# Kernel tuning notes

Hardware: AMD Instinct MI355X
Metric: run time of the kernel (lower is better)

Reference implementation:

```python
import jax, jax.numpy as jnp
import numpy as np

B, NOBJ, QD, VD = 128, 36, 2400, 2048
N = B * NOBJ
NEG_SLOPE = 0.2


def _edges():
    # fully connected per image, self-loops included (PyG GATConv adds them)
    base = np.arange(NOBJ)
    src = np.repeat(base, NOBJ)
    dst = np.tile(base, NOBJ)
    off = (np.arange(B) * NOBJ)[:, None]
    return np.stack([(src[None] + off).reshape(-1), (dst[None] + off).reshape(-1)])


def setup_inputs() -> dict:
    key = jax.random.key(0)
    ks = jax.random.split(key, 24)
    p = lambda k, shape, fan: jax.random.normal(k, shape, jnp.float32) * (1.0 / np.sqrt(fan))
    inp = {
        "question_embedding": jax.random.normal(ks[0], (B, QD), jnp.float32),
        "object_features": jax.random.normal(ks[1], (N, VD), jnp.float32),
        "edge_index": jnp.asarray(_edges(), jnp.int32),
        "Wq": p(ks[2], (QD, 2048), QD), "bq": jnp.zeros((2048,), jnp.float32),
        "Wv": p(ks[3], (VD, 2048), VD), "bv": jnp.zeros((2048,), jnp.float32),
        "W1": p(ks[4], (2048, 4 * 256), 2048), "a1s": p(ks[5], (4, 256), 256),
        "a1d": p(ks[6], (4, 256), 256), "b1": jnp.zeros((1024,), jnp.float32),
        "W2": p(ks[7], (1024, 4 * 256), 1024), "a2s": p(ks[8], (4, 256), 256),
        "a2d": p(ks[9], (4, 256), 256), "b2": jnp.zeros((1024,), jnp.float32),
        "W3": p(ks[10], (1024, 5 * 512), 1024), "a3s": p(ks[11], (5, 512), 512),
        "a3d": p(ks[12], (5, 512), 512), "b3": jnp.zeros((512,), jnp.float32),
        "batch_size": B, "num_obj": NOBJ,
    }
    return inp


def gat_conv(x, edge_index, W, a_src, a_dst, b, heads, ch, concat):
    n = x.shape[0]
    h = (x @ W).reshape(n, heads, ch)                       # [N,H,C]
    src, dst = edge_index[0], edge_index[1]
    al_s = jnp.einsum('nhc,hc->nh', h, a_src)               # [N,H]
    al_d = jnp.einsum('nhc,hc->nh', h, a_dst)
    e = jax.nn.leaky_relu(al_s[src] + al_d[dst], NEG_SLOPE)  # [E,H]
    # segment softmax over edges sharing a destination node
    e_max = jax.ops.segment_max(e, dst, num_segments=n)
    e = jnp.exp(e - e_max[dst])
    denom = jax.ops.segment_sum(e, dst, num_segments=n)
    alpha = e / (denom[dst] + 1e-16)                        # [E,H]
    msg = h[src] * alpha[:, :, None]                        # [E,H,C]
    out = jax.ops.segment_sum(msg, dst, num_segments=n)     # [N,H,C]
    out = out.reshape(n, heads * ch) if concat else out.mean(axis=1)
    return out + b


def reference(question_embedding, object_features, edge_index,
              Wq, bq, Wv, bv,
              W1, a1s, a1d, b1,
              W2, a2s, a2d, b2,
              W3, a3s, a3d, b3,
              batch_size, num_obj):
    # hadamard fusion of question with per-object features
    q = question_embedding @ Wq + bq                        # [B,2048]
    q = jnp.repeat(q, num_obj, axis=0)                      # [N,2048]
    v = object_features @ Wv + bv
    x = q * v
    g1 = jax.nn.relu(gat_conv(x, edge_index, W1, a1s, a1d, b1, 4, 256, True))
    g2 = jax.nn.relu(gat_conv(g1, edge_index, W2, a2s, a2d, b2, 4, 256, True))
    g2 = g2 + g1                                            # residual
    return gat_conv(g2, edge_index, W3, a3s, a3d, b3, 5, 512, False)
```

## Files before the change

### kernel.cpp

```cpp
#include <hip/hip_runtime.h>
#include <hip/hip_bf16.h>

typedef unsigned short u16;
typedef __bf16 bf16x8 __attribute__((ext_vector_type(8)));
typedef float f32x4 __attribute__((ext_vector_type(4)));

#define B_IMG 128
#define NOBJ  36
#define NNODE (B_IMG * NOBJ)

__device__ __forceinline__ float b2f(u16 u) {
    union { unsigned int i; float f; } v; v.i = ((unsigned int)u) << 16; return v.f;
}
__device__ __forceinline__ u16 f2b(float f) {
    union { float f; unsigned int i; } v; v.f = f;
    unsigned int u = v.i;
    return (u16)((u + 0x7fffu + ((u >> 16) & 1u)) >> 16);
}

__global__ __launch_bounds__(256)
void conv_mat(const float* __restrict__ src, u16* __restrict__ dst, int n4) {
    const int i = blockIdx.x * 256 + threadIdx.x;
    if (i >= n4) return;
    const float4 f = ((const float4*)src)[i];
    ushort4 o; o.x = f2b(f.x); o.y = f2b(f.y); o.z = f2b(f.z); o.w = f2b(f.w);
    ((ushort4*)dst)[i] = o;
}

__global__ __launch_bounds__(256)
void conv_pad_qe(const float* __restrict__ src, u16* __restrict__ dst) {
    const int i = blockIdx.x * 256 + threadIdx.x;
    if (i >= 128 * 2560) return;
    const int r = i / 2560, c = i - r * 2560;
    dst[i] = (c < 2400) ? f2b(src[r * 2400 + c]) : (u16)0;
}

__global__ __launch_bounds__(256)
void transpose_cvt(const float* __restrict__ src, u16* __restrict__ dst, int R, int C) {
    __shared__ u16 tile[32][33];
    const int bx = blockIdx.x * 32, by = blockIdx.y * 32;
    const int tx = threadIdx.x & 31, ty = threadIdx.x >> 5;
    #pragma unroll
    for (int i = ty; i < 32; i += 8)
        tile[i][tx] = f2b(src[(size_t)(by + i) * C + bx + tx]);
    __syncthreads();
    #pragma unroll
    for (int i = ty; i < 32; i += 8) dst[(size_t)(bx + i) * R + by + tx] = tile[tx][i];
}

__global__ __launch_bounds__(256)
void transpose_cvt_padK(const float* __restrict__ src, u16* __restrict__ dst) {
    __shared__ u16 tile[32][33];
    const int bx = blockIdx.x * 32, by = blockIdx.y * 32;
    const int tx = threadIdx.x & 31, ty = threadIdx.x >> 5;
    #pragma unroll
    for (int i = ty; i < 32; i += 8) {
        const int k = by + i;
        tile[i][tx] = (k < 2400) ? f2b(src[(size_t)k * 2048 + bx + tx]) : (u16)0;
    }
    __syncthreads();
    #pragma unroll
    for (int i = ty; i < 32; i += 8) dst[(size_t)(bx + i) * 2560 + by + tx] = tile[tx][i];
}

template<int EPI>
__global__ __launch_bounds__(256, 4)
void gemm_tn(const u16* __restrict__ A, const u16* __restrict__ Bt,
             int M, int N, int K, int kLen,
             float* __restrict__ Cf, u16* __restrict__ Cb,
             const float* __restrict__ bias, const float* __restrict__ qmul)
{
    __shared__ __align__(16) u16 lds[2 * 8192];

    const int t    = threadIdx.x;
    const int lane = t & 63;
    const int wave = t >> 6;
    const int wr = wave >> 1, wc = wave & 1;
    const int quad = lane >> 4, l16 = lane & 15;
    const int rowBase = blockIdx.y * 128;
    const int colBase = blockIdx.x * 128;
    const int k0 = blockIdx.z * kLen;

    const u16* gA0 = A  + (size_t)(rowBase + wave * 32 + (lane >> 2)) * K + k0 + (lane & 3) * 8;
    const u16* gA1 = gA0 + 16 * (size_t)K;
    const u16* gB0 = Bt + (size_t)(colBase + wave * 32 + (lane >> 2)) * K + k0 + (lane & 3) * 8;
    const u16* gB1 = gB0 + 16 * (size_t)K;
    const int ro = wave * 1024;

    int afr[4], bfr[4];
    #pragma unroll
    for (int r = 0; r < 4; r++) afr[r] = (wr * 64 + r * 16 + l16) * 32 + quad * 8;
    #pragma unroll
    for (int c = 0; c < 4; c++) bfr[c] = 4096 + (wc * 64 + c * 16 + l16) * 32 + quad * 8;

    f32x4 acc[4][4];
    #pragma unroll
    for (int r = 0; r < 4; r++)
        #pragma unroll
        for (int c = 0; c < 4; c++)
            acc[r][c] = (f32x4){0.f, 0.f, 0.f, 0.f};

    auto gld = [](const u16* g, u16* s) {
        __builtin_amdgcn_global_load_lds(
            (const __attribute__((address_space(1))) void*)g,
            (__attribute__((address_space(3))) void*)s, 16, 0, 0);
    };
    auto dma_stage = [&](int it, int st) {
        const int kk = it * 32;
        const int bo = st * 8192;
        gld(gA0 + kk, &lds[bo + ro]);
        gld(gA1 + kk, &lds[bo + ro + 512]);
        gld(gB0 + kk, &lds[bo + 4096 + ro]);
        gld(gB1 + kk, &lds[bo + 4096 + ro + 512]);
    };

    const int nIter = kLen >> 5;
    dma_stage(0, 0);

    for (int it = 0; it < nIter; ++it) {
        asm volatile("s_waitcnt vmcnt(0)\n\ts_barrier" ::: "memory");
        if (it + 1 < nIter) dma_stage(it + 1, (it + 1) & 1);
        const int bo = (it & 1) * 8192;
        bf16x8 avf[4], bvf[4];
        #pragma unroll
        for (int r = 0; r < 4; r++) avf[r] = *(const bf16x8*)&lds[bo + afr[r]];
        #pragma unroll
        for (int c = 0; c < 4; c++) bvf[c] = *(const bf16x8*)&lds[bo + bfr[c]];
        #pragma unroll
        for (int r = 0; r < 4; r++)
            #pragma unroll
            for (int c = 0; c < 4; c++)
                acc[r][c] = __builtin_amdgcn_mfma_f32_16x16x32_bf16(avf[r], bvf[c], acc[r][c], 0, 0, 0);
    }

    #pragma unroll
    for (int r = 0; r < 4; r++) {
        const int mBase = rowBase + wr * 64 + r * 16 + quad * 4;
        #pragma unroll
        for (int c = 0; c < 4; c++) {
            const int n = colBase + wc * 64 + c * 16 + l16;
            #pragma unroll
            for (int e = 0; e < 4; e++) {
                const int m = mBase + e;
                float v = acc[r][c][e];
                if (EPI == 1) {
                    Cf[((size_t)blockIdx.z * M + m) * N + n] = v;
                } else if (EPI == 2) {
                    v += bias[n];
                    v *= qmul[(size_t)(m / NOBJ) * N + n];
                    Cb[(size_t)m * N + n] = f2b(v);
                } else {
                    Cb[(size_t)m * N + n] = f2b(v);
                }
            }
        }
    }
}

__global__ __launch_bounds__(256)
void qcombine(const float* __restrict__ p, const float* __restrict__ bias,
              float* __restrict__ q, int MN, int S)
{
    const int i = blockIdx.x * 256 + threadIdx.x;
    float s = 0.f;
    for (int z = 0; z < S; z++) s += p[(size_t)z * MN + i];
    q[i] = s + bias[i & 2047];
}

template<int H, int C>
__global__ __launch_bounds__(H * 64)
void al_kernel(const u16* __restrict__ h, const float* __restrict__ a_s,
               const float* __restrict__ a_d, float* __restrict__ als, float* __restrict__ ald)
{
    const int n = blockIdx.x;
    const int wv = threadIdx.x >> 6, lane = threadIdx.x & 63;
    constexpr int PL = C / 64;
    const u16*   hp  = h   + (size_t)n * (H * C) + wv * C + lane * PL;
    const float* asp = a_s + wv * C + lane * PL;
    const float* adp = a_d + wv * C + lane * PL;
    u16 hb[PL];
    if constexpr (PL == 4) { *(uint2*)hb = *(const uint2*)hp; }
    else                   { *(uint4*)hb = *(const uint4*)hp; }
    float s1 = 0.f, s2 = 0.f;
    #pragma unroll
    for (int i = 0; i < PL; i++) {
        const float hv = b2f(hb[i]);
        s1 += hv * asp[i];
        s2 += hv * adp[i];
    }
    #pragma unroll
    for (int off = 32; off > 0; off >>= 1) {
        s1 += __shfl_down(s1, off);
        s2 += __shfl_down(s2, off);
    }
    if (lane == 0) { als[n * H + wv] = s1; ald[n * H + wv] = s2; }
}

template<int H, bool MEAN>
__global__ __launch_bounds__(64)
void alpha_kernel(const float* __restrict__ als, const float* __restrict__ ald,
                  float* __restrict__ alphaG)
{
    __shared__ float asl[36];
    const int b = blockIdx.y, hd = blockIdx.x;
    const int nb = b * NOBJ;
    const int t = threadIdx.x;
    if (t < 36) asl[t] = als[(nb + t) * H + hd];
    __syncthreads();
    if (t >= 36) return;
    const float ad = ald[(nb + t) * H + hd];
    float row[36];
    float mx = -1e30f;
    #pragma unroll
    for (int s = 0; s < 36; s++) {
        float v = asl[s] + ad; v = (v > 0.f) ? v : 0.2f * v;
        row[s] = v; mx = fmaxf(mx, v);
    }
    float sum = 0.f;
    #pragma unroll
    for (int s = 0; s < 36; s++) { row[s] = expf(row[s] - mx); sum += row[s]; }
    const float inv = (MEAN ? 0.2f : 1.0f) / (sum + 1e-16f);
    float* o = alphaG + (((size_t)b * H + hd) * 36 + t) * 36;
    #pragma unroll
    for (int s = 0; s < 36; s++) o[s] = row[s] * inv;
}

template<int H, int C, int MODE>
__global__ __launch_bounds__(192)
void attn_agg(const u16* __restrict__ h, const float* __restrict__ alphaG,
              const float* __restrict__ bias, const u16* __restrict__ resid,
              u16* __restrict__ outb)
{
    constexpr int NSLAB = C / 64;
    __shared__ __align__(16) u16 hl[36 * 64];
    __shared__ float al[36 * 36];
    const int b = blockIdx.y;
    const int hd = blockIdx.x / NSLAB, sl = blockIdx.x - hd * NSLAB;
    const int nb = b * NOBJ, cb = sl * 64;
    const int t = threadIdx.x;

    for (int e = t; e < 36 * 8; e += 192) {
        const int row = e >> 3, col = (e & 7) * 8;
        *(uint4*)&hl[row * 64 + col] =
            *(const uint4*)&h[(size_t)(nb + row) * (H * C) + hd * C + cb + col];
    }
    const float* ap = alphaG + ((size_t)b * H + hd) * 1296;
    for (int e = t; e < 1296; e += 192) al[e] = ap[e];
    __syncthreads();

    #pragma unroll
    for (int p = 0; p < 3; p++) {
        const int e = p * 192 + t;
        const int d = e >> 4, c4 = (e & 15) * 4;
        float a0 = 0, a1 = 0, a2 = 0, a3 = 0;
        for (int s = 0; s < 36; s++) {
            const float av = al[d * 36 + s];
            const ushort4 hv = *(const ushort4*)&hl[s * 64 + c4];
            a0 += av * b2f(hv.x); a1 += av * b2f(hv.y);
            a2 += av * b2f(hv.z); a3 += av * b2f(hv.w);
        }
        const int n = nb + d;
        const size_t base = (size_t)n * (H * C) + hd * C + cb + c4;
        const int bb = hd * C + cb + c4;
        float v0 = a0 + bias[bb + 0];
        float v1 = a1 + bias[bb + 1];
        float v2 = a2 + bias[bb + 2];
        float v3 = a3 + bias[bb + 3];
        v0 = v0 > 0.f ? v0 : 0.f; v1 = v1 > 0.f ? v1 : 0.f;
        v2 = v2 > 0.f ? v2 : 0.f; v3 = v3 > 0.f ? v3 : 0.f;
        if (MODE == 2) {
            v0 += b2f(resid[base + 0]); v1 += b2f(resid[base + 1]);
            v2 += b2f(resid[base + 2]); v3 += b2f(resid[base + 3]);
        }
        outb[base + 0] = f2b(v0); outb[base + 1] = f2b(v1);
        outb[base + 2] = f2b(v2); outb[base + 3] = f2b(v3);
    }
}

__global__ __launch_bounds__(192)
void attn_agg_mean(const u16* __restrict__ h, const float* __restrict__ alphaG,
                   const float* __restrict__ b3, float* __restrict__ outp)
{
    __shared__ __align__(16) u16 hl[36 * 64];
    __shared__ float al[36 * 36];
    const int b = blockIdx.y, sl = blockIdx.x;
    const int nb = b * NOBJ, cb = sl * 64;
    const int t = threadIdx.x;

    float acc[3][4] = {};
    for (int hd = 0; hd < 5; hd++) {
        if (hd) __syncthreads();
        for (int e = t; e < 36 * 8; e += 192) {
            const int row = e >> 3, col = (e & 7) * 8;
            *(uint4*)&hl[row * 64 + col] =
                *(const uint4*)&h[(size_t)(nb + row) * 2560 + hd * 512 + cb + col];
        }
        const float* ap = alphaG + ((size_t)b * 5 + hd) * 1296;
        for (int e = t; e < 1296; e += 192) al[e] = ap[e];
        __syncthreads();
        #pragma unroll
        for (int p = 0; p < 3; p++) {
            const int e = p * 192 + t;
            const int d = e >> 4, c4 = (e & 15) * 4;
            for (int s = 0; s < 36; s++) {
                const float av = al[d * 36 + s];
                const ushort4 hv = *(const ushort4*)&hl[s * 64 + c4];
                acc[p][0] += av * b2f(hv.x); acc[p][1] += av * b2f(hv.y);
                acc[p][2] += av * b2f(hv.z); acc[p][3] += av * b2f(hv.w);
            }
        }
    }
    #pragma unroll
    for (int p = 0; p < 3; p++) {
        const int e = p * 192 + t;
        const int d = e >> 4, c4 = (e & 15) * 4;
        #pragma unroll
        for (int j = 0; j < 4; j++)
            outp[(size_t)(nb + d) * 512 + cb + c4 + j] = acc[p][j] + b3[cb + c4 + j];
    }
}

extern "C" void kernel_launch(void* const* d_in, const int* in_sizes, int n_in,
                              void* d_out, int out_size, void* d_ws, size_t ws_size,
                              hipStream_t stream)
{
    const float* qe  = (const float*)d_in[0];
    const float* of  = (const float*)d_in[1];
    const float* Wq  = (const float*)d_in[3];
    const float* bq  = (const float*)d_in[4];
    const float* Wv  = (const float*)d_in[5];
    const float* bv  = (const float*)d_in[6];
    const float* W1  = (const float*)d_in[7];
    const float* a1s = (const float*)d_in[8];
    const float* a1d = (const float*)d_in[9];
    const float* b1  = (const float*)d_in[10];
    const float* W2  = (const float*)d_in[11];
    const float* a2s = (const float*)d_in[12];
    const float* a2d = (const float*)d_in[13];
    const float* b2  = (const float*)d_in[14];
    const float* W3  = (const float*)d_in[15];
    const float* a3s = (const float*)d_in[16];
    const float* a3d = (const float*)d_in[17];
    const float* b3  = (const float*)d_in[18];
    float* out = (float*)d_out;
    (void)ws_size; (void)in_sizes; (void)n_in; (void)out_size;

    char* W0 = (char*)d_ws;
    size_t off = 0;
    auto alloc = [&](size_t bytes) -> char* {
        char* p = W0 + off; off += (bytes + 255) & ~(size_t)255; return p;
    };
    u16* qe_c = (u16*)alloc(128ull * 2560 * 2);
    u16* of_c = (u16*)alloc(4608ull * 2048 * 2);
    const size_t szA = 4608ull * 2560 * 2;
    const size_t szB = 4608ull * 1024 * 2;
    const size_t szC = 4608ull * 1024 * 2;
    char* Abase = alloc(szA);
    char* Bbase = alloc(szB);
    char* Cbase = alloc(szC);
    char* Dbase = alloc((size_t)NNODE * 5 * 4 * 2);
    float* alphaG = (float*)alloc(128ull * 5 * 36 * 36 * 4);

    u16*   WqT   = (u16*)Abase;
    float* qpart = (float*)(Abase + 2048ull * 2560 * 2);
    u16*   x     = (u16*)Abase;
    u16*   g1    = (u16*)Abase;
    u16*   h3    = (u16*)Abase;
    u16*   WvT   = (u16*)Bbase;
    float* q     = (float*)(Bbase + 2048ull * 2048 * 2);
    u16*   W1T   = (u16*)Bbase;
    u16*   W2T   = (u16*)Bbase;
    u16*   g2    = (u16*)Bbase;
    u16*   h1    = (u16*)Cbase;
    u16*   h2    = (u16*)Cbase;
    u16*   W3T   = (u16*)Cbase;
    float* als   = (float*)Dbase;
    float* ald   = (float*)(Dbase + (size_t)NNODE * 5 * 4);

    conv_pad_qe<<<(128 * 2560 + 255) / 256, 256, 0, stream>>>(qe, qe_c);
    conv_mat<<<(4608 * 2048 / 4 + 255) / 256, 256, 0, stream>>>(of, of_c, 4608 * 2048 / 4);

    transpose_cvt_padK<<<dim3(64, 80), 256, 0, stream>>>(Wq, WqT);
    gemm_tn<1><<<dim3(16, 1, 5), 256, 0, stream>>>(qe_c, WqT, 128, 2048, 2560, 512,
                                                   qpart, nullptr, nullptr, nullptr);
    qcombine<<<dim3(128 * 2048 / 256), 256, 0, stream>>>(qpart, bq, q, 128 * 2048, 5);

    transpose_cvt<<<dim3(64, 64), 256, 0, stream>>>(Wv, WvT, 2048, 2048);
    gemm_tn<2><<<dim3(16, 36, 1), 256, 0, stream>>>(of_c, WvT, 4608, 2048, 2048, 2048,
                                                    nullptr, x, bv, q);

    transpose_cvt<<<dim3(32, 64), 256, 0, stream>>>(W1, W1T, 2048, 1024);
    gemm_tn<0><<<dim3(8, 36, 1), 256, 0, stream>>>(x, W1T, 4608, 1024, 2048, 2048,
                                                   nullptr, h1, nullptr, nullptr);
    al_kernel<4, 256><<<dim3(NNODE), 256, 0, stream>>>(h1, a1s, a1d, als, ald);
    alpha_kernel<4, false><<<dim3(4, B_IMG), 64, 0, stream>>>(als, ald, alphaG);
    attn_agg<4, 256, 1><<<dim3(16, B_IMG), 192, 0, stream>>>(h1, alphaG, b1, nullptr, g1);

    transpose_cvt<<<dim3(32, 32), 256, 0, stream>>>(W2, W2T, 1024, 1024);
    gemm_tn<0><<<dim3(8, 36, 1), 256, 0, stream>>>(g1, W2T, 4608, 1024, 1024, 1024,
                                                   nullptr, h2, nullptr, nullptr);
    al_kernel<4, 256><<<dim3(NNODE), 256, 0, stream>>>(h2, a2s, a2d, als, ald);
    alpha_kernel<4, false><<<dim3(4, B_IMG), 64, 0, stream>>>(als, ald, alphaG);
    attn_agg<4, 256, 2><<<dim3(16, B_IMG), 192, 0, stream>>>(h2, alphaG, b2, g1, g2);

    transpose_cvt<<<dim3(80, 32), 256, 0, stream>>>(W3, W3T, 1024, 2560);
    gemm_tn<0><<<dim3(20, 36, 1), 256, 0, stream>>>(g2, W3T, 4608, 2560, 1024, 1024,
                                                    nullptr, h3, nullptr, nullptr);
    al_kernel<5, 512><<<dim3(NNODE), 320, 0, stream>>>(h3, a3s, a3d, als, ald);
    alpha_kernel<5, true><<<dim3(5, B_IMG), 64, 0, stream>>>(als, ald, alphaG);
    attn_agg_mean<<<dim3(8, B_IMG), 192, 0, stream>>>(h3, alphaG, b3, out);
}
```

Measured before the change: 475.9 us.

## Triple-buffer GEMM with swizzled LDS, fuse conversion, transpose and attention-logit kernels

The GEMM moves from double to triple buffering, with a deeper prefetch and a partial vmcnt wait, so global loads overlap more with MFMA work. Its LDS layout is XOR-swizzled to reduce bank conflicts on fragment reads. The separate conversion and transpose kernels are merged into combined launches (W1/W2, Wq/Wv), and the per-node logit kernel is fused with the softmax alpha kernel, cutting launch count and intermediate buffers. Occupancy drops from 4 to 3 blocks per CU because of the extra LDS, and W2T now gets a separate workspace region so it can be transposed early.

```diff
diff --git a/kernel.cpp b/kernel.cpp
--- a/kernel.cpp
+++ b/kernel.cpp
@@ -19,58 +19,55 @@
 }
 
 __global__ __launch_bounds__(256)
-void conv_mat(const float* __restrict__ src, u16* __restrict__ dst, int n4) {
-    const int i = blockIdx.x * 256 + threadIdx.x;
-    if (i >= n4) return;
-    const float4 f = ((const float4*)src)[i];
-    ushort4 o; o.x = f2b(f.x); o.y = f2b(f.y); o.z = f2b(f.z); o.w = f2b(f.w);
-    ((ushort4*)dst)[i] = o;
+void conv_all(const float* __restrict__ of, u16* __restrict__ of_c,
+              const float* __restrict__ qe, u16* __restrict__ qe_c)
+{
+    const int bid = blockIdx.x;
+    if (bid < 9216) {
+        const int i = bid * 256 + threadIdx.x;
+        const float4 f = ((const float4*)of)[i];
+        ushort4 o; o.x = f2b(f.x); o.y = f2b(f.y); o.z = f2b(f.z); o.w = f2b(f.w);
+        ((ushort4*)of_c)[i] = o;
+    } else {
+        const int i = (bid - 9216) * 256 + threadIdx.x;
+        const int r = i / 2560, c = i - r * 2560;
+        qe_c[i] = (c < 2400) ? f2b(qe[r * 2400 + c]) : (u16)0;
+    }
 }
 
 __global__ __launch_bounds__(256)
-void conv_pad_qe(const float* __restrict__ src, u16* __restrict__ dst) {
-    const int i = blockIdx.x * 256 + threadIdx.x;
-    if (i >= 128 * 2560) return;
-    const int r = i / 2560, c = i - r * 2560;
-    dst[i] = (c < 2400) ? f2b(src[r * 2400 + c]) : (u16)0;
-}
-
-__global__ __launch_bounds__(256)
-void transpose_cvt(const float* __restrict__ src, u16* __restrict__ dst, int R, int C) {
+void transpose_cvt2(const float* __restrict__ s0, u16* __restrict__ d0,
+                    int Rs0, int Rd0, int C0, int nt0,
+                    const float* __restrict__ s1, u16* __restrict__ d1,
+                    int Rs1, int Rd1, int C1)
+{
     __shared__ u16 tile[32][33];
-    const int bx = blockIdx.x * 32, by = blockIdx.y * 32;
-    const int tx = threadIdx.x & 31, ty = threadIdx.x >> 5;
-    #pragma unroll
-    for (int i = ty; i < 32; i += 8)
-        tile[i][tx] = f2b(src[(size_t)(by + i) * C + bx + tx]);
+    int tb = blockIdx.x;
+    const float* src; u16* dst; int Rs, Rd, C;
+    if (tb < nt0) { src = s0; dst = d0; Rs = Rs0; Rd = Rd0; C = C0; }
+    else { tb -= nt0; src = s1; dst = d1; Rs = Rs1; Rd = Rd1; C = C1; }
+    const int ntx = C >> 5;
+    const int ty = tb / ntx, tx = tb - ty * ntx;
+    const int bx = tx * 32, by = ty * 32;
+    const int lx = threadIdx.x & 31, ly = threadIdx.x >> 5;
+    #pragma unroll
+    for (int i = ly; i < 32; i += 8) {
+        const int k = by + i;
+        tile[i][lx] = (k < Rs) ? f2b(src[(size_t)k * C + bx + lx]) : (u16)0;
+    }
     __syncthreads();
     #pragma unroll
-    for (int i = ty; i < 32; i += 8) dst[(size_t)(bx + i) * R + by + tx] = tile[tx][i];
-}
-
-__global__ __launch_bounds__(256)
-void transpose_cvt_padK(const float* __restrict__ src, u16* __restrict__ dst) {
-    __shared__ u16 tile[32][33];
-    const int bx = blockIdx.x * 32, by = blockIdx.y * 32;
-    const int tx = threadIdx.x & 31, ty = threadIdx.x >> 5;
-    #pragma unroll
-    for (int i = ty; i < 32; i += 8) {
-        const int k = by + i;
-        tile[i][tx] = (k < 2400) ? f2b(src[(size_t)k * 2048 + bx + tx]) : (u16)0;
-    }
-    __syncthreads();
-    #pragma unroll
-    for (int i = ty; i < 32; i += 8) dst[(size_t)(bx + i) * 2560 + by + tx] = tile[tx][i];
+    for (int i = ly; i < 32; i += 8) dst[(size_t)(bx + i) * Rd + by + lx] = tile[lx][i];
 }
 
 template<int EPI>
-__global__ __launch_bounds__(256, 4)
+__global__ __launch_bounds__(256, 3)
 void gemm_tn(const u16* __restrict__ A, const u16* __restrict__ Bt,
              int M, int N, int K, int kLen,
              float* __restrict__ Cf, u16* __restrict__ Cb,
              const float* __restrict__ bias, const float* __restrict__ qmul)
 {
-    __shared__ __align__(16) u16 lds[2 * 8192];
+    __shared__ __align__(16) u16 lds[3 * 8192];
 
     const int t    = threadIdx.x;
     const int lane = t & 63;
@@ -81,17 +78,19 @@
     const int colBase = blockIdx.x * 128;
     const int k0 = blockIdx.z * kLen;
 
-    const u16* gA0 = A  + (size_t)(rowBase + wave * 32 + (lane >> 2)) * K + k0 + (lane & 3) * 8;
+    const int lq = (lane & 3) ^ ((lane >> 3) & 3);
+    const u16* gA0 = A  + (size_t)(rowBase + wave * 32 + (lane >> 2)) * K + k0 + lq * 8;
     const u16* gA1 = gA0 + 16 * (size_t)K;
-    const u16* gB0 = Bt + (size_t)(colBase + wave * 32 + (lane >> 2)) * K + k0 + (lane & 3) * 8;
+    const u16* gB0 = Bt + (size_t)(colBase + wave * 32 + (lane >> 2)) * K + k0 + lq * 8;
     const u16* gB1 = gB0 + 16 * (size_t)K;
     const int ro = wave * 1024;
 
+    const int sw = (quad ^ ((l16 >> 1) & 3)) * 8;
     int afr[4], bfr[4];
     #pragma unroll
-    for (int r = 0; r < 4; r++) afr[r] = (wr * 64 + r * 16 + l16) * 32 + quad * 8;
-    #pragma unroll
-    for (int c = 0; c < 4; c++) bfr[c] = 4096 + (wc * 64 + c * 16 + l16) * 32 + quad * 8;
+    for (int r = 0; r < 4; r++) afr[r] = (wr * 64 + r * 16 + l16) * 32 + sw;
+    #pragma unroll
+    for (int c = 0; c < 4; c++) bfr[c] = 4096 + (wc * 64 + c * 16 + l16) * 32 + sw;
 
     f32x4 acc[4][4];
     #pragma unroll
@@ -116,11 +115,13 @@
 
     const int nIter = kLen >> 5;
     dma_stage(0, 0);
-
+    dma_stage(1, 1);
+    int st = 0, st2 = 2;
     for (int it = 0; it < nIter; ++it) {
-        asm volatile("s_waitcnt vmcnt(0)\n\ts_barrier" ::: "memory");
-        if (it + 1 < nIter) dma_stage(it + 1, (it + 1) & 1);
-        const int bo = (it & 1) * 8192;
+        if (it + 1 < nIter) asm volatile("s_waitcnt vmcnt(4)\n\ts_barrier" ::: "memory");
+        else                asm volatile("s_waitcnt vmcnt(0)\n\ts_barrier" ::: "memory");
+        if (it + 2 < nIter) dma_stage(it + 2, st2);
+        const int bo = st * 8192;
         bf16x8 avf[4], bvf[4];
         #pragma unroll
         for (int r = 0; r < 4; r++) avf[r] = *(const bf16x8*)&lds[bo + afr[r]];
@@ -131,6 +132,8 @@
             #pragma unroll
             for (int c = 0; c < 4; c++)
                 acc[r][c] = __builtin_amdgcn_mfma_f32_16x16x32_bf16(avf[r], bvf[c], acc[r][c], 0, 0, 0);
+        st  = (st  == 2) ? 0 : st  + 1;
+        st2 = (st2 == 2) ? 0 : st2 + 1;
     }
 
     #pragma unroll
@@ -167,48 +170,40 @@
     q[i] = s + bias[i & 2047];
 }
 
-template<int H, int C>
-__global__ __launch_bounds__(H * 64)
-void al_kernel(const u16* __restrict__ h, const float* __restrict__ a_s,
-               const float* __restrict__ a_d, float* __restrict__ als, float* __restrict__ ald)
-{
-    const int n = blockIdx.x;
-    const int wv = threadIdx.x >> 6, lane = threadIdx.x & 63;
+template<int H, int C, bool MEAN>
+__global__ __launch_bounds__(256)
+void al_alpha(const u16* __restrict__ h, const float* __restrict__ a_s,
+              const float* __restrict__ a_d, float* __restrict__ alphaG)
+{
+    __shared__ float asl[36], adl[36];
+    const int hd = blockIdx.x, b = blockIdx.y;
+    const int nb = b * NOBJ;
+    const int t = threadIdx.x, wv = t >> 6, lane = t & 63;
     constexpr int PL = C / 64;
-    const u16*   hp  = h   + (size_t)n * (H * C) + wv * C + lane * PL;
-    const float* asp = a_s + wv * C + lane * PL;
-    const float* adp = a_d + wv * C + lane * PL;
-    u16 hb[PL];
-    if constexpr (PL == 4) { *(uint2*)hb = *(const uint2*)hp; }
-    else                   { *(uint4*)hb = *(const uint4*)hp; }
-    float s1 = 0.f, s2 = 0.f;
-    #pragma unroll
-    for (int i = 0; i < PL; i++) {
-        const float hv = b2f(hb[i]);
-        s1 += hv * asp[i];
-        s2 += hv * adp[i];
-    }
-    #pragma unroll
-    for (int off = 32; off > 0; off >>= 1) {
-        s1 += __shfl_down(s1, off);
-        s2 += __shfl_down(s2, off);
-    }
-    if (lane == 0) { als[n * H + wv] = s1; ald[n * H + wv] = s2; }
-}
-
-template<int H, bool MEAN>
-__global__ __launch_bounds__(64)
-void alpha_kernel(const float* __restrict__ als, const float* __restrict__ ald,
-                  float* __restrict__ alphaG)
-{
-    __shared__ float asl[36];
-    const int b = blockIdx.y, hd = blockIdx.x;
-    const int nb = b * NOBJ;
-    const int t = threadIdx.x;
-    if (t < 36) asl[t] = als[(nb + t) * H + hd];
+    const float* asp = a_s + hd * C + lane * PL;
+    const float* adp = a_d + hd * C + lane * PL;
+    for (int n = wv; n < 36; n += 4) {
+        const u16* hp = h + (size_t)(nb + n) * (H * C) + hd * C + lane * PL;
+        u16 hb[PL];
+        if constexpr (PL == 4) { *(uint2*)hb = *(const uint2*)hp; }
+        else                   { *(uint4*)hb = *(const uint4*)hp; }
+        float s1 = 0.f, s2 = 0.f;
+        #pragma unroll
+        for (int i = 0; i < PL; i++) {
+            const float hv = b2f(hb[i]);
+            s1 += hv * asp[i];
+            s2 += hv * adp[i];
+        }
+        #pragma unroll
+        for (int off = 32; off > 0; off >>= 1) {
+            s1 += __shfl_down(s1, off);
+            s2 += __shfl_down(s2, off);
+        }
+        if (lane == 0) { asl[n] = s1; adl[n] = s2; }
+    }
     __syncthreads();
     if (t >= 36) return;
-    const float ad = ald[(nb + t) * H + hd];
+    const float ad = adl[t];
     float row[36];
     float mx = -1e30f;
     #pragma unroll
@@ -358,7 +353,6 @@
     char* Abase = alloc(szA);
     char* Bbase = alloc(szB);
     char* Cbase = alloc(szC);
-    char* Dbase = alloc((size_t)NNODE * 5 * 4 * 2);
     float* alphaG = (float*)alloc(128ull * 5 * 36 * 36 * 4);
 
     u16*   WqT   = (u16*)Abase;
@@ -369,44 +363,44 @@
     u16*   WvT   = (u16*)Bbase;
     float* q     = (float*)(Bbase + 2048ull * 2048 * 2);
     u16*   W1T   = (u16*)Bbase;
-    u16*   W2T   = (u16*)Bbase;
+    u16*   W2T   = (u16*)(Bbase + 1024ull * 2048 * 2);
     u16*   g2    = (u16*)Bbase;
     u16*   h1    = (u16*)Cbase;
     u16*   h2    = (u16*)Cbase;
     u16*   W3T   = (u16*)Cbase;
-    float* als   = (float*)Dbase;
-    float* ald   = (float*)(Dbase + (size_t)NNODE * 5 * 4);
-
-    conv_pad_qe<<<(128 * 2560 + 255) / 256, 256, 0, stream>>>(qe, qe_c);
-    conv_mat<<<(4608 * 2048 / 4 + 255) / 256, 256, 0, stream>>>(of, of_c, 4608 * 2048 / 4);
-
-    transpose_cvt_padK<<<dim3(64, 80), 256, 0, stream>>>(Wq, WqT);
+
+    conv_all<<<dim3(9216 + 1280), 256, 0, stream>>>(of, of_c, qe, qe_c);
+
+    transpose_cvt2<<<dim3(5120 + 4096), 256, 0, stream>>>(
+        Wq, WqT, 2400, 2560, 2048, 5120,
+        Wv, WvT, 2048, 2048, 2048);
+
     gemm_tn<1><<<dim3(16, 1, 5), 256, 0, stream>>>(qe_c, WqT, 128, 2048, 2560, 512,
                                                    qpart, nullptr, nullptr, nullptr);
     qcombine<<<dim3(128 * 2048 / 256), 256, 0, stream>>>(qpart, bq, q, 128 * 2048, 5);
 
-    transpose_cvt<<<dim3(64, 64), 256, 0, stream>>>(Wv, WvT, 2048, 2048);
     gemm_tn<2><<<dim3(16, 36, 1), 256, 0, stream>>>(of_c, WvT, 4608, 2048, 2048, 2048,
                                                     nullptr, x, bv, q);
 
-    transpose_cvt<<<dim3(32, 64), 256, 0, stream>>>(W1, W1T, 2048, 1024);
+    transpose_cvt2<<<dim3(2048 + 1024), 256, 0, stream>>>(
+        W1, W1T, 2048, 2048, 1024, 2048,
+        W2, W2T, 1024, 1024, 1024);
+
     gemm_tn<0><<<dim3(8, 36, 1), 256, 0, stream>>>(x, W1T, 4608, 1024, 2048, 2048,
                                                    nullptr, h1, nullptr, nullptr);
-    al_kernel<4, 256><<<dim3(NNODE), 256, 0, stream>>>(h1, a1s, a1d, als, ald);
-    alpha_kernel<4, false><<<dim3(4, B_IMG), 64, 0, stream>>>(als, ald, alphaG);
+    al_alpha<4, 256, false><<<dim3(4, B_IMG), 256, 0, stream>>>(h1, a1s, a1d, alphaG);
     attn_agg<4, 256, 1><<<dim3(16, B_IMG), 192, 0, stream>>>(h1, alphaG, b1, nullptr, g1);
 
-    transpose_cvt<<<dim3(32, 32), 256, 0, stream>>>(W2, W2T, 1024, 1024);
     gemm_tn<0><<<dim3(8, 36, 1), 256, 0, stream>>>(g1, W2T, 4608, 1024, 1024, 1024,
                                                    nullptr, h2, nullptr, nullptr);
-    al_kernel<4, 256><<<dim3(NNODE), 256, 0, stream>>>(h2, a2s, a2d, als, ald);
-    alpha_kernel<4, false><<<dim3(4, B_IMG), 64, 0, stream>>>(als, ald, alphaG);
+    al_alpha<4, 256, false><<<dim3(4, B_IMG), 256, 0, stream>>>(h2, a2s, a2d, alphaG);
     attn_agg<4, 256, 2><<<dim3(16, B_IMG), 192, 0, stream>>>(h2, alphaG, b2, g1, g2);
 
-    transpose_cvt<<<dim3(80, 32), 256, 0, stream>>>(W3, W3T, 1024, 2560);
+    transpose_cvt2<<<dim3(2560), 256, 0, stream>>>(
+        W3, W3T, 1024, 1024, 2560, 2560,
+        W3, W3T, 1024, 1024, 2560);
     gemm_tn<0><<<dim3(20, 36, 1), 256, 0, stream>>>(g2, W3T, 4608, 2560, 1024, 1024,
                                                     nullptr, h3, nullptr, nullptr);
-    al_kernel<5, 512><<<dim3(NNODE), 320, 0, stream>>>(h3, a3s, a3d, als, ald);
-    alpha_kernel<5, true><<<dim3(5, B_IMG), 64, 0, stream>>>(als, ald, alphaG);
+    al_alpha<5, 512, true><<<dim3(5, B_IMG), 256, 0, stream>>>(h3, a3s, a3d, alphaG);
     attn_agg_mean<<<dim3(8, B_IMG), 192, 0, stream>>>(h3, alphaG, b3, out);
 }
```

New measurement: 478.6 us. About the same (+0.6%).
